# Performance work log

Hardware: AMD Instinct MI355X
Metric: run time of the kernel (lower is better)

## Reference

```python
import jax, jax.numpy as jnp
import numpy as np

DIM, D_STATE, D_CONV, EXPAND = 512, 16, 4, 2
D_INNER = EXPAND * DIM            # 1024
DT_RANK = (DIM + 15) // 16        # 32
B, L = 2, 2048


def setup_inputs() -> dict:
    key = jax.random.key(0)
    ks = jax.random.split(key, 12)
    s_in = 1.0 / np.sqrt(DIM)
    s_xp = 1.0 / np.sqrt(D_INNER)
    s_dt = 1.0 / np.sqrt(DT_RANK)
    return {
        "x": jax.random.normal(ks[0], (B, L, DIM), jnp.float32),
        "ln_g": jnp.ones((DIM,), jnp.float32),
        "ln_b": jnp.zeros((DIM,), jnp.float32),
        "W_in": jax.random.normal(ks[1], (2 * D_INNER, DIM), jnp.float32) * s_in,
        "conv_w": jax.random.normal(ks[2], (D_INNER, D_CONV), jnp.float32) * 0.5,
        "conv_b": jax.random.normal(ks[3], (D_INNER,), jnp.float32) * 0.1,
        "W_xproj": jax.random.normal(ks[4], (DT_RANK + 2 * D_STATE, D_INNER), jnp.float32) * s_xp,
        "W_dt": jax.random.normal(ks[5], (D_INNER, DT_RANK), jnp.float32) * s_dt,
        "b_dt": jax.random.normal(ks[6], (D_INNER,), jnp.float32) * 0.1 - 4.0,  # softplus -> small dt
        "A_log": jnp.log(jax.random.uniform(ks[7], (D_INNER, D_STATE), jnp.float32, 1.0, 16.0)),
        "Dp": jax.random.normal(ks[8], (D_INNER,), jnp.float32),
        "W_out": jax.random.normal(ks[9], (DIM, D_INNER), jnp.float32) * s_xp,
    }


def _layernorm(x, g, b, eps=1e-5):
    mu = jnp.mean(x, -1, keepdims=True)
    var = jnp.mean(jnp.square(x - mu), -1, keepdims=True)
    return (x - mu) * jax.lax.rsqrt(var + eps) * g + b


def reference(x, ln_g, ln_b, W_in, conv_w, conv_b, W_xproj, W_dt, b_dt, A_log, Dp, W_out):
    h = _layernorm(x, ln_g, ln_b)
    # input projection -> [B,L,2*d_inner]
    xz = jnp.einsum('bld,ed->ble', h, W_in)
    xp, z = jnp.split(xz, 2, axis=-1)
    # depthwise causal conv1d over time (kernel d_conv), then SiLU
    xp_pad = jnp.pad(xp, ((0, 0), (D_CONV - 1, 0), (0, 0)))
    xc = conv_b
    for k in range(D_CONV):
        xc = xc + xp_pad[:, k:k + L, :] * conv_w[:, k]
    xc = jax.nn.silu(xc)
    # x_proj -> dt, B, C
    proj = jnp.einsum('bld,ed->ble', xc, W_xproj)
    dt_r = proj[..., :DT_RANK]
    Bm = proj[..., DT_RANK:DT_RANK + D_STATE]          # [B,L,n]
    Cm = proj[..., DT_RANK + D_STATE:]                 # [B,L,n]
    dt = jax.nn.softplus(jnp.einsum('blr,dr->bld', dt_r, W_dt) + b_dt)  # [B,L,d]
    A = -jnp.exp(A_log)                                # [d,n]
    dA = jnp.exp(jnp.einsum('bld,dn->bldn', dt, A))    # [B,L,d,n]
    dBx = dt[..., None] * Bm[:, :, None, :] * xc[..., None]  # [B,L,d,n]
    # selective scan over time (time-major for lax.scan)
    def step(s, inp):
        dA_t, dBx_t, C_t = inp
        s = s * dA_t + dBx_t                           # [B,d,n]
        y_t = jnp.einsum('bdn,bn->bd', s, C_t)
        return s, y_t
    s0 = jnp.zeros((B, D_INNER, D_STATE), xc.dtype)
    _, ys = jax.lax.scan(step, s0,
                         (jnp.moveaxis(dA, 1, 0), jnp.moveaxis(dBx, 1, 0), jnp.moveaxis(Cm, 1, 0)))
    y = jnp.moveaxis(ys, 0, 1)                         # [B,L,d]
    y = y + xc * Dp
    y = y * jax.nn.silu(z)
    out = jnp.einsum('bld,ed->ble', y, W_out)
    return x + out  # dropout is identity in eval mode
```

## Files before the change

### kernel.cpp

```cpp
#include <hip/hip_runtime.h>
#include <hip/hip_bf16.h>
#include <math.h>

#define B_      2
#define L_      2048
#define DIM_    512
#define DINNER  1024
#define DTRANK  32
#define DSTATE  16
#define DCONV   4
#define BL      (B_ * L_)
#define NCHUNK  64
#define CLEN    (L_ / NCHUNK)

typedef __attribute__((ext_vector_type(8))) short bf16x8;
typedef __attribute__((ext_vector_type(4))) float f32x4;

static __device__ __forceinline__ unsigned short f2bf(float f) {
  __hip_bfloat16 h = __float2bfloat16(f);
  return *(unsigned short*)&h;
}
static __device__ __forceinline__ float bf2f(unsigned short u) {
  return __uint_as_float(((unsigned int)u) << 16);
}

__global__ __launch_bounds__(256) void cvt_ln_kernel(
    const float* __restrict__ s0, const float* __restrict__ s1,
    const float* __restrict__ s2, __hip_bfloat16* __restrict__ d0,
    __hip_bfloat16* __restrict__ d1, __hip_bfloat16* __restrict__ d2,
    const float* __restrict__ x, const float* __restrict__ g,
    const float* __restrict__ b, __hip_bfloat16* __restrict__ h) {
  int blk = blockIdx.x;
  if (blk < 1600) {
    int i = (blk * 256 + threadIdx.x) * 4;
    const float* s; __hip_bfloat16* d; int off;
    if (i < 1048576)            { s = s0; d = d0; off = i; }
    else if (i < 1048576+65536) { s = s1; d = d1; off = i - 1048576; }
    else                        { s = s2; d = d2; off = i - 1114112; }
    float4 v = *(const float4*)(s + off);
    d[off + 0] = __float2bfloat16(v.x);
    d[off + 1] = __float2bfloat16(v.y);
    d[off + 2] = __float2bfloat16(v.z);
    d[off + 3] = __float2bfloat16(v.w);
    return;
  }
  int row = (blk - 1600) * 4 + (threadIdx.x >> 6);
  int lane = threadIdx.x & 63;
  const float* xr = x + (size_t)row * DIM_;
  float v[8];
  float sum = 0.f;
#pragma unroll
  for (int i = 0; i < 8; i++) { v[i] = xr[lane + i * 64]; sum += v[i]; }
#pragma unroll
  for (int o = 32; o > 0; o >>= 1) sum += __shfl_xor(sum, o, 64);
  float mu = sum * (1.f / DIM_);
  float vs = 0.f;
#pragma unroll
  for (int i = 0; i < 8; i++) { float dd = v[i] - mu; vs += dd * dd; }
#pragma unroll
  for (int o = 32; o > 0; o >>= 1) vs += __shfl_xor(vs, o, 64);
  float rstd = rsqrtf(vs * (1.f / DIM_) + 1e-5f);
  __hip_bfloat16* hr = h + (size_t)row * DIM_;
#pragma unroll
  for (int i = 0; i < 8; i++) {
    int c = lane + i * 64;
    hr[c] = __float2bfloat16((v[i] - mu) * rstd * g[c] + b[c]);
  }
}

template <bool ADD_RES, bool OUT_BF16>
__global__ __launch_bounds__(256) void gemm_mfma_128(
    const __hip_bfloat16* __restrict__ A, int lda,
    const __hip_bfloat16* __restrict__ Bw, int ldb,
    const float* __restrict__ Res, int ldr,
    void* __restrict__ C, int ldc, int K) {
  constexpr int LDL = 72;
  __shared__ short As[128 * LDL];
  __shared__ short Bs[128 * LDL];
  int t = threadIdx.x;
  int n0 = blockIdx.x * 128, m0 = blockIdx.y * 128;
  int w = t >> 6, lane = t & 63;
  int wm = (w >> 1) * 64, wn = (w & 1) * 64;
  int l15 = lane & 15, quad = lane >> 4;
  int srow = t >> 3, scol = (t & 7) * 8;
  const short* Ag = (const short*)A + (size_t)(m0 + srow) * lda + scol;
  const short* Bg = (const short*)Bw + (size_t)(n0 + srow) * ldb + scol;
  f32x4 acc[4][4];
#pragma unroll
  for (int i = 0; i < 4; i++)
#pragma unroll
    for (int j = 0; j < 4; j++) acc[i][j] = (f32x4){0.f, 0.f, 0.f, 0.f};
  for (int k0 = 0; k0 < K; k0 += 64) {
    __syncthreads();
#pragma unroll
    for (int p = 0; p < 4; p++) {
      *(bf16x8*)&As[(srow + p * 32) * LDL + scol] =
          *(const bf16x8*)(Ag + (size_t)(p * 32) * lda + k0);
      *(bf16x8*)&Bs[(srow + p * 32) * LDL + scol] =
          *(const bf16x8*)(Bg + (size_t)(p * 32) * ldb + k0);
    }
    __syncthreads();
#pragma unroll
    for (int kk = 0; kk < 64; kk += 32) {
      bf16x8 af[4], bfr[4];
#pragma unroll
      for (int i = 0; i < 4; i++) {
        af[i] = *(const bf16x8*)&As[(wm + i * 16 + l15) * LDL + kk + quad * 8];
        bfr[i] = *(const bf16x8*)&Bs[(wn + i * 16 + l15) * LDL + kk + quad * 8];
      }
#pragma unroll
      for (int i = 0; i < 4; i++)
#pragma unroll
        for (int j = 0; j < 4; j++)
          acc[i][j] = __builtin_amdgcn_mfma_f32_16x16x32_bf16(
              af[i], bfr[j], acc[i][j], 0, 0, 0);
    }
  }
#pragma unroll
  for (int i = 0; i < 4; i++)
#pragma unroll
    for (int r = 0; r < 4; r++) {
      int row = m0 + wm + i * 16 + quad * 4 + r;
#pragma unroll
      for (int j = 0; j < 4; j++) {
        int col = n0 + wn + j * 16 + l15;
        float v = acc[i][j][r];
        if (ADD_RES) v += Res[(size_t)row * ldr + col];
        if (OUT_BF16)
          ((unsigned short*)C)[(size_t)row * ldc + col] = f2bf(v);
        else
          ((float*)C)[(size_t)row * ldc + col] = v;
      }
    }
}

__global__ __launch_bounds__(256) void gemm_mfma_64(
    const __hip_bfloat16* __restrict__ A, int lda,
    const __hip_bfloat16* __restrict__ Bw, int ldb,
    float* __restrict__ C, int ldc, int K, size_t czs) {
  constexpr int LDL = 72;
  __shared__ short As[64 * LDL];
  __shared__ short Bs[64 * LDL];
  int t = threadIdx.x;
  int n0 = blockIdx.x * 64, m0 = blockIdx.y * 64;
  size_t kbase = (size_t)blockIdx.z * K;
  int w = t >> 6, lane = t & 63;
  int wm = (w >> 1) * 32, wn = (w & 1) * 32;
  int l15 = lane & 15, quad = lane >> 4;
  int srow = t >> 3, scol = (t & 7) * 8;
  const short* Ag = (const short*)A + (size_t)(m0 + srow) * lda + scol + kbase;
  const short* Bg = (const short*)Bw + (size_t)(n0 + srow) * ldb + scol + kbase;
  f32x4 acc[2][2];
#pragma unroll
  for (int i = 0; i < 2; i++)
#pragma unroll
    for (int j = 0; j < 2; j++) acc[i][j] = (f32x4){0.f, 0.f, 0.f, 0.f};
  for (int k0 = 0; k0 < K; k0 += 64) {
    __syncthreads();
#pragma unroll
    for (int p = 0; p < 2; p++) {
      *(bf16x8*)&As[(srow + p * 32) * LDL + scol] =
          *(const bf16x8*)(Ag + (size_t)(p * 32) * lda + k0);
      *(bf16x8*)&Bs[(srow + p * 32) * LDL + scol] =
          *(const bf16x8*)(Bg + (size_t)(p * 32) * ldb + k0);
    }
    __syncthreads();
#pragma unroll
    for (int kk = 0; kk < 64; kk += 32) {
      bf16x8 af[2], bfr[2];
#pragma unroll
      for (int i = 0; i < 2; i++) {
        af[i] = *(const bf16x8*)&As[(wm + i * 16 + l15) * LDL + kk + quad * 8];
        bfr[i] = *(const bf16x8*)&Bs[(wn + i * 16 + l15) * LDL + kk + quad * 8];
      }
#pragma unroll
      for (int i = 0; i < 2; i++)
#pragma unroll
        for (int j = 0; j < 2; j++)
          acc[i][j] = __builtin_amdgcn_mfma_f32_16x16x32_bf16(
              af[i], bfr[j], acc[i][j], 0, 0, 0);
    }
  }
  float* Cz = C + czs * blockIdx.z;
#pragma unroll
  for (int i = 0; i < 2; i++)
#pragma unroll
    for (int r = 0; r < 4; r++) {
      int row = m0 + wm + i * 16 + quad * 4 + r;
#pragma unroll
      for (int j = 0; j < 2; j++) {
        int col = n0 + wn + j * 16 + l15;
        Cz[(size_t)row * ldc + col] = acc[i][j][r];
      }
    }
}

__global__ __launch_bounds__(256) void reduce4_kernel(
    const float* __restrict__ pp, float* __restrict__ proj) {
  int i = blockIdx.x * 256 + threadIdx.x;
  proj[i] = pp[i] + pp[i + 262144] + pp[i + 2 * 262144] + pp[i + 3 * 262144];
}

__global__ __launch_bounds__(256) void conv_silu_kernel(
    unsigned short* __restrict__ xzb, const float* __restrict__ cw,
    const float* __restrict__ cb, __hip_bfloat16* __restrict__ xc_bf) {
  int idx = blockIdx.x * 256 + threadIdx.x;
  int d4 = (idx & 255) * 4;
  int bl = idx >> 8;
  int l = bl & (L_ - 1);
  unsigned short* base = xzb + (size_t)bl * 2048 + d4;
  float4 acc = *(const float4*)(cb + d4);
  float4 w0 = *(const float4*)(cw + (d4 + 0) * 4);
  float4 w1 = *(const float4*)(cw + (d4 + 1) * 4);
  float4 w2 = *(const float4*)(cw + (d4 + 2) * 4);
  float4 w3 = *(const float4*)(cw + (d4 + 3) * 4);
  if (l >= 3) {
    ushort4 r = *(const ushort4*)(base - 3 * 2048);
    acc.x += bf2f(r.x) * w0.x; acc.y += bf2f(r.y) * w1.x;
    acc.z += bf2f(r.z) * w2.x; acc.w += bf2f(r.w) * w3.x;
  }
  if (l >= 2) {
    ushort4 r = *(const ushort4*)(base - 2 * 2048);
    acc.x += bf2f(r.x) * w0.y; acc.y += bf2f(r.y) * w1.y;
    acc.z += bf2f(r.z) * w2.y; acc.w += bf2f(r.w) * w3.y;
  }
  if (l >= 1) {
    ushort4 r = *(const ushort4*)(base - 1 * 2048);
    acc.x += bf2f(r.x) * w0.z; acc.y += bf2f(r.y) * w1.z;
    acc.z += bf2f(r.z) * w2.z; acc.w += bf2f(r.w) * w3.z;
  }
  {
    ushort4 r = *(const ushort4*)(base);
    acc.x += bf2f(r.x) * w0.w; acc.y += bf2f(r.y) * w1.w;
    acc.z += bf2f(r.z) * w2.w; acc.w += bf2f(r.w) * w3.w;
  }
  float4 v;
  v.x = acc.x / (1.f + __expf(-acc.x));
  v.y = acc.y / (1.f + __expf(-acc.y));
  v.z = acc.z / (1.f + __expf(-acc.z));
  v.w = acc.w / (1.f + __expf(-acc.w));
  ushort4 hb;
  hb.x = f2bf(v.x); hb.y = f2bf(v.y); hb.z = f2bf(v.z); hb.w = f2bf(v.w);
  *(ushort4*)(xc_bf + (size_t)bl * DINNER + d4) = hb;
  ushort4 zu = *(const ushort4*)(base + DINNER);
  float z0 = bf2f(zu.x), z1 = bf2f(zu.y), z2 = bf2f(zu.z), z3 = bf2f(zu.w);
  ushort4 gu;
  gu.x = f2bf(z0 / (1.f + __expf(-z0)));
  gu.y = f2bf(z1 / (1.f + __expf(-z1)));
  gu.z = f2bf(z2 / (1.f + __expf(-z2)));
  gu.w = f2bf(z3 / (1.f + __expf(-z3)));
  *(ushort4*)(base + DINNER) = gu;
}

__global__ __launch_bounds__(256) void dt_kernel(
    const float* __restrict__ proj, const float* __restrict__ Wdt,
    const float* __restrict__ bdt, float* __restrict__ dt) {
  int blk = blockIdx.x;
  int dgrp = blk & 3;
  int bl0 = (blk >> 2) * 16;
  int d = dgrp * 256 + threadIdx.x;
  __shared__ float pr[16 * 32];
  for (int i = threadIdx.x; i < 16 * 32; i += 256) {
    int row = i >> 5, col = i & 31;
    pr[i] = proj[(size_t)(bl0 + row) * 64 + col];
  }
  float w[32];
#pragma unroll
  for (int r4 = 0; r4 < 8; r4++) {
    float4 wv = *(const float4*)(Wdt + (size_t)d * 32 + r4 * 4);
    w[r4 * 4 + 0] = wv.x; w[r4 * 4 + 1] = wv.y;
    w[r4 * 4 + 2] = wv.z; w[r4 * 4 + 3] = wv.w;
  }
  float bias = bdt[d];
  __syncthreads();
  for (int row = 0; row < 16; row++) {
    float acc = bias;
#pragma unroll
    for (int r4 = 0; r4 < 8; r4++) {
      float4 pv = *(const float4*)&pr[row * 32 + r4 * 4];
      acc += pv.x * w[r4 * 4 + 0] + pv.y * w[r4 * 4 + 1] +
             pv.z * w[r4 * 4 + 2] + pv.w * w[r4 * 4 + 3];
    }
    float sp = (acc > 20.f) ? acc : log1pf(__expf(acc));
    dt[(size_t)(bl0 + row) * DINNER + d] = sp;
  }
}

__global__ __launch_bounds__(256) void scan1_kernel(
    const float* __restrict__ dt, const __hip_bfloat16* __restrict__ xc_bf,
    const float* __restrict__ proj, const float* __restrict__ A_log,
    float* __restrict__ T, float* __restrict__ E) {
  int bid = blockIdx.x;
  int dgrp = bid & 63;
  int c = (bid >> 6) & (NCHUNK - 1);
  int b = bid >> 12;
  int n = threadIdx.x & 15;
  int d = dgrp * 16 + (threadIdx.x >> 4);
  float Aa = -__expf(A_log[(size_t)d * 16 + n]);
  float Tn = 1.f, En = 0.f;
  int l0 = c * CLEN;
  for (int l = l0; l < l0 + CLEN; l++) {
    int bl = b * L_ + l;
    float dtv = dt[(size_t)bl * DINNER + d];
    float xv = __bfloat162float(xc_bf[(size_t)bl * DINNER + d]);
    float Bv = proj[(size_t)bl * 64 + 32 + n];
    float dA = __expf(dtv * Aa);
    Tn *= dA;
    En = En * dA + dtv * xv * Bv;
  }
  size_t o = (((size_t)b * NCHUNK + c) * DINNER + d) * 16 + n;
  T[o] = Tn; E[o] = En;
}

__global__ __launch_bounds__(256) void combine_kernel(
    float* __restrict__ T, const float* __restrict__ E) {
  int idx = blockIdx.x * 256 + threadIdx.x;
  int b = idx >> 14;
  int dn = idx & 16383;
  size_t base = (size_t)b * NCHUNK * (DINNER * 16) + dn;
  float s = 0.f;
#pragma unroll
  for (int batch = 0; batch < 4; batch++) {
    float t[16], e[16];
#pragma unroll
    for (int j = 0; j < 16; j++) {
      size_t o = base + (size_t)(batch * 16 + j) * (DINNER * 16);
      t[j] = T[o]; e[j] = E[o];
    }
#pragma unroll
    for (int j = 0; j < 16; j++) {
      T[base + (size_t)(batch * 16 + j) * (DINNER * 16)] = s;
      s = t[j] * s + e[j];
    }
  }
}

__global__ __launch_bounds__(256) void scan2_kernel(
    const float* __restrict__ dt, const __hip_bfloat16* __restrict__ xc_bf,
    const float* __restrict__ proj, const float* __restrict__ A_log,
    const float* __restrict__ Sstart, const float* __restrict__ Dp,
    unsigned short* __restrict__ xzb) {
  int bid = blockIdx.x;
  int dgrp = bid & 3;
  int c = (bid >> 2) & (NCHUNK - 1);
  int b = bid >> 8;
  int d = dgrp * 256 + threadIdx.x;
  int l0 = c * CLEN;
  __shared__ float Bs[CLEN * 16];
  __shared__ float Cs[CLEN * 16];
  for (int i = threadIdx.x; i < CLEN * 16; i += 256) {
    int row = i >> 4, nn = i & 15;
    const float* pr = proj + (size_t)(b * L_ + l0 + row) * 64;
    Bs[i] = pr[32 + nn];
    Cs[i] = pr[48 + nn];
  }
  float Aa[16], s[16];
  size_t sb = (((size_t)b * NCHUNK + c) * DINNER + d) * 16;
#pragma unroll
  for (int q = 0; q < 4; q++) {
    float4 av = *(const float4*)(A_log + (size_t)d * 16 + q * 4);
    Aa[q * 4 + 0] = -__expf(av.x); Aa[q * 4 + 1] = -__expf(av.y);
    Aa[q * 4 + 2] = -__expf(av.z); Aa[q * 4 + 3] = -__expf(av.w);
    float4 sv = *(const float4*)(Sstart + sb + q * 4);
    s[q * 4 + 0] = sv.x; s[q * 4 + 1] = sv.y;
    s[q * 4 + 2] = sv.z; s[q * 4 + 3] = sv.w;
  }
  float Dv = Dp[d];
  __syncthreads();
  for (int l = l0; l < l0 + CLEN; l++) {
    int bl = b * L_ + l;
    float dtv = dt[(size_t)bl * DINNER + d];
    float xv = __bfloat162float(xc_bf[(size_t)bl * DINNER + d]);
    float dx = dtv * xv;
    int lrow = (l - l0) * 16;
    float y = 0.f;
#pragma unroll
    for (int n = 0; n < 16; n++) {
      float dA = __expf(dtv * Aa[n]);
      s[n] = s[n] * dA + dx * Bs[lrow + n];
      y += s[n] * Cs[lrow + n];
    }
    float gate = bf2f(xzb[(size_t)bl * 2048 + 1024 + d]);
    xzb[(size_t)bl * 2048 + d] = f2bf((y + xv * Dv) * gate);
  }
}

extern "C" void kernel_launch(void* const* d_in, const int* in_sizes, int n_in,
                              void* d_out, int out_size, void* d_ws, size_t ws_size,
                              hipStream_t stream) {
  const float* x      = (const float*)d_in[0];
  const float* ln_g   = (const float*)d_in[1];
  const float* ln_b   = (const float*)d_in[2];
  const float* W_in   = (const float*)d_in[3];
  const float* conv_w = (const float*)d_in[4];
  const float* conv_b = (const float*)d_in[5];
  const float* W_xprj = (const float*)d_in[6];
  const float* W_dt   = (const float*)d_in[7];
  const float* b_dt   = (const float*)d_in[8];
  const float* A_log  = (const float*)d_in[9];
  const float* Dp     = (const float*)d_in[10];
  const float* W_out  = (const float*)d_in[11];
  float* out = (float*)d_out;

  float* ws     = (float*)d_ws;
  float* xzb_f  = ws;
  float* xcbf_f = xzb_f + 4194304;
  float* proj   = xcbf_f + 2097152;
  float* dtb    = proj + 262144;
  float* T      = dtb + 4194304;
  float* E      = T + 2097152;
  float* hbf_f  = E + 2097152;
  float* wbf    = hbf_f + 1048576;

  unsigned short* xzb   = (unsigned short*)xzb_f;
  __hip_bfloat16* xc_bf = (__hip_bfloat16*)xcbf_f;
  float* pp = dtb;
  __hip_bfloat16* h_bf  = (__hip_bfloat16*)hbf_f;
  __hip_bfloat16* Wb_in = (__hip_bfloat16*)wbf;
  __hip_bfloat16* Wb_xp = Wb_in + 1048576;
  __hip_bfloat16* Wb_out = Wb_xp + 65536;
  __hip_bfloat16* y_bf  = (__hip_bfloat16*)xzb;

  cvt_ln_kernel<<<1600 + BL / 4, 256, 0, stream>>>(
      W_in, W_xprj, W_out, Wb_in, Wb_xp, Wb_out, x, ln_g, ln_b, h_bf);
  gemm_mfma_128<false, true><<<dim3(2 * DINNER / 128, BL / 128), 256, 0, stream>>>(
      h_bf, DIM_, Wb_in, DIM_, nullptr, 0, xzb, 2 * DINNER, DIM_);
  conv_silu_kernel<<<(BL * DINNER / 4) / 256, 256, 0, stream>>>(
      xzb, conv_w, conv_b, xc_bf);
  gemm_mfma_64<<<dim3(1, BL / 64, 4), 256, 0, stream>>>(
      xc_bf, DINNER, Wb_xp, DINNER, pp, 64, 256, 262144);
  reduce4_kernel<<<1024, 256, 0, stream>>>(pp, proj);
  dt_kernel<<<(BL / 16) * 4, 256, 0, stream>>>(proj, W_dt, b_dt, dtb);
  scan1_kernel<<<B_ * NCHUNK * 64, 256, 0, stream>>>(dtb, xc_bf, proj, A_log, T, E);
  combine_kernel<<<(B_ * DINNER * 16) / 256, 256, 0, stream>>>(T, E);
  scan2_kernel<<<B_ * NCHUNK * 4, 256, 0, stream>>>(dtb, xc_bf, proj, A_log, T, Dp, xzb);
  gemm_mfma_128<true, false><<<dim3(DIM_ / 128, BL / 128), 256, 0, stream>>>(
      y_bf, 2048, Wb_out, DINNER, x, DIM_, out, DIM_, DINNER);
}
```

Before: 236.2 us.

## Use direct global-to-LDS loads in GEMMs, fuse reductions and gating, stage scan1 inputs

```diff
diff --git a/kernel.cpp b/kernel.cpp
--- a/kernel.cpp
+++ b/kernel.cpp
@@ -22,6 +22,12 @@
 }
 static __device__ __forceinline__ float bf2f(unsigned short u) {
   return __uint_as_float(((unsigned int)u) << 16);
+}
+
+static __device__ __forceinline__ void gload16(const void* g, void* l) {
+  __builtin_amdgcn_global_load_lds(
+      (const __attribute__((address_space(1))) void*)g,
+      (__attribute__((address_space(3))) void*)l, 16, 0, 0);
 }
 
 __global__ __launch_bounds__(256) void cvt_ln_kernel(
@@ -74,17 +80,16 @@
     const __hip_bfloat16* __restrict__ Bw, int ldb,
     const float* __restrict__ Res, int ldr,
     void* __restrict__ C, int ldc, int K) {
-  constexpr int LDL = 72;
-  __shared__ short As[128 * LDL];
-  __shared__ short Bs[128 * LDL];
+  __shared__ short As[128 * 64];
+  __shared__ short Bs[128 * 64];
   int t = threadIdx.x;
   int n0 = blockIdx.x * 128, m0 = blockIdx.y * 128;
   int w = t >> 6, lane = t & 63;
   int wm = (w >> 1) * 64, wn = (w & 1) * 64;
   int l15 = lane & 15, quad = lane >> 4;
-  int srow = t >> 3, scol = (t & 7) * 8;
-  const short* Ag = (const short*)A + (size_t)(m0 + srow) * lda + scol;
-  const short* Bg = (const short*)Bw + (size_t)(n0 + srow) * ldb + scol;
+  int lr = lane >> 3, lc = (lane & 7) * 8;
+  const short* Ag = (const short*)A + (size_t)(m0 + w * 32 + lr) * lda + lc;
+  const short* Bg = (const short*)Bw + (size_t)(n0 + w * 32 + lr) * ldb + lc;
   f32x4 acc[4][4];
 #pragma unroll
   for (int i = 0; i < 4; i++)
@@ -94,10 +99,8 @@
     __syncthreads();
 #pragma unroll
     for (int p = 0; p < 4; p++) {
-      *(bf16x8*)&As[(srow + p * 32) * LDL + scol] =
-          *(const bf16x8*)(Ag + (size_t)(p * 32) * lda + k0);
-      *(bf16x8*)&Bs[(srow + p * 32) * LDL + scol] =
-          *(const bf16x8*)(Bg + (size_t)(p * 32) * ldb + k0);
+      gload16(Ag + (size_t)(p * 8) * lda + k0, &As[(w * 32 + p * 8) * 64]);
+      gload16(Bg + (size_t)(p * 8) * ldb + k0, &Bs[(w * 32 + p * 8) * 64]);
     }
     __syncthreads();
 #pragma unroll
@@ -105,8 +108,8 @@
       bf16x8 af[4], bfr[4];
 #pragma unroll
       for (int i = 0; i < 4; i++) {
-        af[i] = *(const bf16x8*)&As[(wm + i * 16 + l15) * LDL + kk + quad * 8];
-        bfr[i] = *(const bf16x8*)&Bs[(wn + i * 16 + l15) * LDL + kk + quad * 8];
+        af[i] = *(const bf16x8*)&As[(wm + i * 16 + l15) * 64 + kk + quad * 8];
+        bfr[i] = *(const bf16x8*)&Bs[(wn + i * 16 + l15) * 64 + kk + quad * 8];
       }
 #pragma unroll
       for (int i = 0; i < 4; i++)
@@ -134,22 +137,23 @@
     }
 }
 
+template <bool ADD_RES>
 __global__ __launch_bounds__(256) void gemm_mfma_64(
     const __hip_bfloat16* __restrict__ A, int lda,
     const __hip_bfloat16* __restrict__ Bw, int ldb,
+    const float* __restrict__ Res, int ldr,
     float* __restrict__ C, int ldc, int K, size_t czs) {
-  constexpr int LDL = 72;
-  __shared__ short As[64 * LDL];
-  __shared__ short Bs[64 * LDL];
+  __shared__ short As[64 * 64];
+  __shared__ short Bs[64 * 64];
   int t = threadIdx.x;
   int n0 = blockIdx.x * 64, m0 = blockIdx.y * 64;
   size_t kbase = (size_t)blockIdx.z * K;
   int w = t >> 6, lane = t & 63;
   int wm = (w >> 1) * 32, wn = (w & 1) * 32;
   int l15 = lane & 15, quad = lane >> 4;
-  int srow = t >> 3, scol = (t & 7) * 8;
-  const short* Ag = (const short*)A + (size_t)(m0 + srow) * lda + scol + kbase;
-  const short* Bg = (const short*)Bw + (size_t)(n0 + srow) * ldb + scol + kbase;
+  int lr = lane >> 3, lc = (lane & 7) * 8;
+  const short* Ag = (const short*)A + (size_t)(m0 + w * 16 + lr) * lda + lc + kbase;
+  const short* Bg = (const short*)Bw + (size_t)(n0 + w * 16 + lr) * ldb + lc + kbase;
   f32x4 acc[2][2];
 #pragma unroll
   for (int i = 0; i < 2; i++)
@@ -159,10 +163,8 @@
     __syncthreads();
 #pragma unroll
     for (int p = 0; p < 2; p++) {
-      *(bf16x8*)&As[(srow + p * 32) * LDL + scol] =
-          *(const bf16x8*)(Ag + (size_t)(p * 32) * lda + k0);
-      *(bf16x8*)&Bs[(srow + p * 32) * LDL + scol] =
-          *(const bf16x8*)(Bg + (size_t)(p * 32) * ldb + k0);
+      gload16(Ag + (size_t)(p * 8) * lda + k0, &As[(w * 16 + p * 8) * 64]);
+      gload16(Bg + (size_t)(p * 8) * ldb + k0, &Bs[(w * 16 + p * 8) * 64]);
     }
     __syncthreads();
 #pragma unroll
@@ -170,8 +172,8 @@
       bf16x8 af[2], bfr[2];
 #pragma unroll
       for (int i = 0; i < 2; i++) {
-        af[i] = *(const bf16x8*)&As[(wm + i * 16 + l15) * LDL + kk + quad * 8];
-        bfr[i] = *(const bf16x8*)&Bs[(wn + i * 16 + l15) * LDL + kk + quad * 8];
+        af[i] = *(const bf16x8*)&As[(wm + i * 16 + l15) * 64 + kk + quad * 8];
+        bfr[i] = *(const bf16x8*)&Bs[(wn + i * 16 + l15) * 64 + kk + quad * 8];
       }
 #pragma unroll
       for (int i = 0; i < 2; i++)
@@ -190,25 +192,21 @@
 #pragma unroll
       for (int j = 0; j < 2; j++) {
         int col = n0 + wn + j * 16 + l15;
-        Cz[(size_t)row * ldc + col] = acc[i][j][r];
+        float v = acc[i][j][r];
+        if (ADD_RES) v += Res[(size_t)row * ldr + col];
+        Cz[(size_t)row * ldc + col] = v;
       }
     }
 }
 
-__global__ __launch_bounds__(256) void reduce4_kernel(
-    const float* __restrict__ pp, float* __restrict__ proj) {
-  int i = blockIdx.x * 256 + threadIdx.x;
-  proj[i] = pp[i] + pp[i + 262144] + pp[i + 2 * 262144] + pp[i + 3 * 262144];
-}
-
 __global__ __launch_bounds__(256) void conv_silu_kernel(
-    unsigned short* __restrict__ xzb, const float* __restrict__ cw,
+    const unsigned short* __restrict__ xzb, const float* __restrict__ cw,
     const float* __restrict__ cb, __hip_bfloat16* __restrict__ xc_bf) {
   int idx = blockIdx.x * 256 + threadIdx.x;
   int d4 = (idx & 255) * 4;
   int bl = idx >> 8;
   int l = bl & (L_ - 1);
-  unsigned short* base = xzb + (size_t)bl * 2048 + d4;
+  const unsigned short* base = xzb + (size_t)bl * 2048 + d4;
   float4 acc = *(const float4*)(cb + d4);
   float4 w0 = *(const float4*)(cw + (d4 + 0) * 4);
   float4 w1 = *(const float4*)(cw + (d4 + 1) * 4);
@@ -242,27 +240,22 @@
   ushort4 hb;
   hb.x = f2bf(v.x); hb.y = f2bf(v.y); hb.z = f2bf(v.z); hb.w = f2bf(v.w);
   *(ushort4*)(xc_bf + (size_t)bl * DINNER + d4) = hb;
-  ushort4 zu = *(const ushort4*)(base + DINNER);
-  float z0 = bf2f(zu.x), z1 = bf2f(zu.y), z2 = bf2f(zu.z), z3 = bf2f(zu.w);
-  ushort4 gu;
-  gu.x = f2bf(z0 / (1.f + __expf(-z0)));
-  gu.y = f2bf(z1 / (1.f + __expf(-z1)));
-  gu.z = f2bf(z2 / (1.f + __expf(-z2)));
-  gu.w = f2bf(z3 / (1.f + __expf(-z3)));
-  *(ushort4*)(base + DINNER) = gu;
 }
 
 __global__ __launch_bounds__(256) void dt_kernel(
-    const float* __restrict__ proj, const float* __restrict__ Wdt,
-    const float* __restrict__ bdt, float* __restrict__ dt) {
+    const float* __restrict__ pp, float* __restrict__ proj,
+    const float* __restrict__ Wdt, const float* __restrict__ bdt,
+    float* __restrict__ dt) {
   int blk = blockIdx.x;
   int dgrp = blk & 3;
   int bl0 = (blk >> 2) * 16;
   int d = dgrp * 256 + threadIdx.x;
-  __shared__ float pr[16 * 32];
-  for (int i = threadIdx.x; i < 16 * 32; i += 256) {
-    int row = i >> 5, col = i & 31;
-    pr[i] = proj[(size_t)(bl0 + row) * 64 + col];
+  __shared__ float pr[16 * 64];
+  for (int i = threadIdx.x; i < 16 * 64; i += 256) {
+    size_t o = (size_t)bl0 * 64 + i;
+    float v = pp[o] + pp[o + 262144] + pp[o + 2 * 262144] + pp[o + 3 * 262144];
+    pr[i] = v;
+    if (dgrp == 0) proj[o] = v;
   }
   float w[32];
 #pragma unroll
@@ -277,7 +270,7 @@
     float acc = bias;
 #pragma unroll
     for (int r4 = 0; r4 < 8; r4++) {
-      float4 pv = *(const float4*)&pr[row * 32 + r4 * 4];
+      float4 pv = *(const float4*)&pr[row * 64 + r4 * 4];
       acc += pv.x * w[r4 * 4 + 0] + pv.y * w[r4 * 4 + 1] +
              pv.z * w[r4 * 4 + 2] + pv.w * w[r4 * 4 + 3];
     }
@@ -294,19 +287,31 @@
   int dgrp = bid & 63;
   int c = (bid >> 6) & (NCHUNK - 1);
   int b = bid >> 12;
-  int n = threadIdx.x & 15;
-  int d = dgrp * 16 + (threadIdx.x >> 4);
+  int tid = threadIdx.x;
+  int n = tid & 15;
+  int dl = tid >> 4;
+  int d = dgrp * 16 + dl;
+  int l0 = c * CLEN;
+  __shared__ float dts[CLEN * 16];
+  __shared__ float dxs[CLEN * 16];
+  __shared__ float Bsh[CLEN * 16];
+  for (int i = tid; i < CLEN * 16; i += 256) {
+    int row = i >> 4, col = i & 15;
+    size_t bl = (size_t)(b * L_ + l0 + row);
+    float dtv = dt[bl * DINNER + dgrp * 16 + col];
+    float xv = __bfloat162float(xc_bf[bl * DINNER + dgrp * 16 + col]);
+    dts[i] = dtv;
+    dxs[i] = dtv * xv;
+    Bsh[i] = proj[bl * 64 + 32 + col];
+  }
   float Aa = -__expf(A_log[(size_t)d * 16 + n]);
+  __syncthreads();
   float Tn = 1.f, En = 0.f;
-  int l0 = c * CLEN;
-  for (int l = l0; l < l0 + CLEN; l++) {
-    int bl = b * L_ + l;
-    float dtv = dt[(size_t)bl * DINNER + d];
-    float xv = __bfloat162float(xc_bf[(size_t)bl * DINNER + d]);
-    float Bv = proj[(size_t)bl * 64 + 32 + n];
-    float dA = __expf(dtv * Aa);
+#pragma unroll 8
+  for (int l = 0; l < CLEN; l++) {
+    float dA = __expf(dts[l * 16 + dl] * Aa);
     Tn *= dA;
-    En = En * dA + dtv * xv * Bv;
+    En = En * dA + dxs[l * 16 + dl] * Bsh[l * 16 + n];
   }
   size_t o = (((size_t)b * NCHUNK + c) * DINNER + d) * 16 + n;
   T[o] = Tn; E[o] = En;
@@ -380,7 +385,8 @@
       s[n] = s[n] * dA + dx * Bs[lrow + n];
       y += s[n] * Cs[lrow + n];
     }
-    float gate = bf2f(xzb[(size_t)bl * 2048 + 1024 + d]);
+    float zv = bf2f(xzb[(size_t)bl * 2048 + 1024 + d]);
+    float gate = zv / (1.f + __expf(-zv));
     xzb[(size_t)bl * 2048 + d] = f2bf((y + xv * Dv) * gate);
   }
 }
@@ -406,7 +412,8 @@
   float* xzb_f  = ws;
   float* xcbf_f = xzb_f + 4194304;
   float* proj   = xcbf_f + 2097152;
-  float* dtb    = proj + 262144;
+  float* pp     = proj + 262144;
+  float* dtb    = pp + 1048576;
   float* T      = dtb + 4194304;
   float* E      = T + 2097152;
   float* hbf_f  = E + 2097152;
@@ -414,7 +421,6 @@
 
   unsigned short* xzb   = (unsigned short*)xzb_f;
   __hip_bfloat16* xc_bf = (__hip_bfloat16*)xcbf_f;
-  float* pp = dtb;
   __hip_bfloat16* h_bf  = (__hip_bfloat16*)hbf_f;
   __hip_bfloat16* Wb_in = (__hip_bfloat16*)wbf;
   __hip_bfloat16* Wb_xp = Wb_in + 1048576;
@@ -427,13 +433,12 @@
       h_bf, DIM_, Wb_in, DIM_, nullptr, 0, xzb, 2 * DINNER, DIM_);
   conv_silu_kernel<<<(BL * DINNER / 4) / 256, 256, 0, stream>>>(
       xzb, conv_w, conv_b, xc_bf);
-  gemm_mfma_64<<<dim3(1, BL / 64, 4), 256, 0, stream>>>(
-      xc_bf, DINNER, Wb_xp, DINNER, pp, 64, 256, 262144);
-  reduce4_kernel<<<1024, 256, 0, stream>>>(pp, proj);
-  dt_kernel<<<(BL / 16) * 4, 256, 0, stream>>>(proj, W_dt, b_dt, dtb);
+  gemm_mfma_64<false><<<dim3(1, BL / 64, 4), 256, 0, stream>>>(
+      xc_bf, DINNER, Wb_xp, DINNER, nullptr, 0, pp, 64, 256, 262144);
+  dt_kernel<<<(BL / 16) * 4, 256, 0, stream>>>(pp, proj, W_dt, b_dt, dtb);
   scan1_kernel<<<B_ * NCHUNK * 64, 256, 0, stream>>>(dtb, xc_bf, proj, A_log, T, E);
   combine_kernel<<<(B_ * DINNER * 16) / 256, 256, 0, stream>>>(T, E);
   scan2_kernel<<<B_ * NCHUNK * 4, 256, 0, stream>>>(dtb, xc_bf, proj, A_log, T, Dp, xzb);
-  gemm_mfma_128<true, false><<<dim3(DIM_ / 128, BL / 128), 256, 0, stream>>>(
-      y_bf, 2048, Wb_out, DINNER, x, DIM_, out, DIM_, DINNER);
-}
+  gemm_mfma_64<true><<<dim3(DIM_ / 64, BL / 64, 1), 256, 0, stream>>>(
+      y_bf, 2048, Wb_out, DINNER, x, DIM_, out, DIM_, DINNER, 0);
+}
```

Result: faster. 220.6 us (-6.6%).
